# Performance work log

Hardware: AMD Instinct MI355X
Metric: run time of the kernel (lower is better)

The kernel has to match this reference:

```python
import jax, jax.numpy as jnp
import numpy as np

H = 1024      # hidden_size
V = 32000     # output_size (vocab)
L = 512       # max_length (encoder positions)
B = 256       # batch


def setup_inputs() -> dict:
    key = jax.random.key(0)
    ks = jax.random.split(key, 12)
    s = 0.02
    return {
        "input": jax.random.randint(ks[0], (B,), 0, V),
        "hidden": jax.random.normal(ks[1], (1, B, H), jnp.float32),
        "encoder_outputs": jax.random.normal(ks[2], (L, H), jnp.float32),
        # learned params (PyTorch layout: Linear weight is [out, in])
        "emb": jax.random.normal(ks[3], (V, H), jnp.float32) * s,
        "attn_W": jax.random.normal(ks[4], (L, 2 * H), jnp.float32) * s,
        "attn_b": jnp.zeros((L,), jnp.float32),
        "comb_W": jax.random.normal(ks[5], (H, 2 * H), jnp.float32) * s,
        "comb_b": jnp.zeros((H,), jnp.float32),
        "W_ih": jax.random.normal(ks[6], (3 * H, H), jnp.float32) * s,
        "W_hh": jax.random.normal(ks[7], (3 * H, H), jnp.float32) * s,
        "b_ih": jnp.zeros((3 * H,), jnp.float32),
        "b_hh": jnp.zeros((3 * H,), jnp.float32),
        "out_W": jax.random.normal(ks[8], (V, H), jnp.float32) * s,
        "out_b": jnp.zeros((V,), jnp.float32),
    }


def reference(input, hidden, encoder_outputs, emb, attn_W, attn_b,
              comb_W, comb_b, W_ih, W_hh, b_ih, b_hh, out_W, out_b):
    h = hidden[0]                                   # [B,H]
    embedded = emb[input]                           # [B,H] (dropout in eval mode = identity)
    attn_logits = jnp.concatenate([embedded, h], axis=1) @ attn_W.T + attn_b
    attn_weights = jax.nn.softmax(attn_logits, axis=1)        # [B,L]
    attn_applied = attn_weights @ encoder_outputs              # [B,H]
    x = jnp.concatenate([embedded, attn_applied], axis=1) @ comb_W.T + comb_b
    x = jax.nn.relu(x)                                         # [B,H]
    # single-step GRU (PyTorch gate layout: r, z, n)
    gi = x @ W_ih.T + b_ih                                     # [B,3H]
    gh = h @ W_hh.T + b_hh                                     # [B,3H]
    gi_r, gi_z, gi_n = jnp.split(gi, 3, axis=1)
    gh_r, gh_z, gh_n = jnp.split(gh, 3, axis=1)
    r = jax.nn.sigmoid(gi_r + gh_r)
    z = jax.nn.sigmoid(gi_z + gh_z)
    n = jnp.tanh(gi_n + r * gh_n)
    h_new = (1.0 - z) * n + z * h                              # [B,H]
    output = jax.nn.log_softmax(h_new @ out_W.T + out_b, axis=1)  # [B,V]
    return output, h_new[None], attn_weights
```

## Files before the change

kernel.cpp:

```cpp
#include <hip/hip_runtime.h>
#include <hip/hip_bf16.h>
#include <cstdint>

#define DEVI __device__ __forceinline__

typedef __bf16 bf16x8 __attribute__((ext_vector_type(8)));
typedef float  f32x4  __attribute__((ext_vector_type(4)));

constexpr int Hdim = 1024;
constexpr int Vdim = 32000;
constexpr int Ldim = 512;
constexpr int Bdim = 256;

DEVI unsigned short f2bf(float f) {
  __bf16 h = (__bf16)f;
  return __builtin_bit_cast(unsigned short, h);
}

constexpr int FP4 = 36;

__global__ __launch_bounds__(1024, 4)
void gemm_flat5(const unsigned short* __restrict__ A,
                const float* __restrict__ W,
                const float* __restrict__ bias,
                float* __restrict__ C,
                float2* __restrict__ plse)
{
  __shared__ unsigned short lW[4][128 * FP4];

  const int t    = threadIdx.x;
  const int lane = t & 63;
  const int wv   = t >> 6;
  const int r16  = lane & 15;
  const int k8   = (lane >> 4) * 8;
  const int n0   = blockIdx.x * 128;

  const int srow = t >> 3;
  const int stc  = (t & 7) * 4;

  const float*          Wb = W + (size_t)(n0 + srow) * 1024 + stc;
  const unsigned short* Ab = A + (size_t)(wv * 16 + r16) * 1024 + k8;

  f32x4 acc[8];
#pragma unroll
  for (int n = 0; n < 8; ++n)
#pragma unroll
    for (int r = 0; r < 4; ++r) acc[n][r] = 0.f;

  f32x4 w0_, w1_;
  uint4 a0_, a1_, a2_, a3_;

#define LOADW(RW, KT) RW = *reinterpret_cast<const f32x4*>(Wb + (KT) * 32)
#define LOADA(RA, KT) RA = *reinterpret_cast<const uint4*>(Ab + (KT) * 32)

#define STOREW(RW, BUF) do {                                                   \
    ushort4 u_;                                                                \
    u_.x = f2bf(RW[0]); u_.y = f2bf(RW[1]);                                    \
    u_.z = f2bf(RW[2]); u_.w = f2bf(RW[3]);                                    \
    *reinterpret_cast<ushort4*>(&lW[BUF][srow * FP4 + stc]) = u_;              \
  } while (0)

#define COMP(RA, BUF) do {                                                     \
    _Pragma("unroll")                                                          \
    for (int n = 0; n < 8; ++n) {                                              \
      bf16x8 bw_ = *reinterpret_cast<const bf16x8*>(                           \
          &lW[BUF][(n * 16 + r16) * FP4 + k8]);                                \
      acc[n] = __builtin_amdgcn_mfma_f32_16x16x32_bf16(                        \
          __builtin_bit_cast(bf16x8, RA), bw_, acc[n], 0, 0, 0);               \
    }                                                                          \
  } while (0)

  LOADW(w0_, 0); LOADW(w1_, 1);
  LOADA(a0_, 0); LOADA(a1_, 1); LOADA(a2_, 2); LOADA(a3_, 3);
  STOREW(w0_, 0); LOADW(w0_, 2);
  STOREW(w1_, 1); LOADW(w1_, 3);
  __syncthreads();

  for (int kt = 0; kt < 32; kt += 4) {
    COMP(a0_, 0);
    STOREW(w0_, 2);
    { const int kn = (kt + 4 < 32) ? kt + 4 : 31; LOADW(w0_, kn); LOADA(a0_, kn); }
    __syncthreads();

    COMP(a1_, 1);
    STOREW(w1_, 3);
    { const int kn = (kt + 5 < 32) ? kt + 5 : 31; LOADW(w1_, kn); LOADA(a1_, kn); }
    __syncthreads();

    COMP(a2_, 2);
    STOREW(w0_, 0);
    { const int kn = (kt + 6 < 32) ? kt + 6 : 31; LOADW(w0_, kn); LOADA(a2_, kn); }
    __syncthreads();

    COMP(a3_, 3);
    STOREW(w1_, 1);
    { const int kn = (kt + 7 < 32) ? kt + 7 : 31; LOADW(w1_, kn); LOADA(a3_, kn); }
    __syncthreads();
  }

#undef COMP
#undef STOREW
#undef LOADA
#undef LOADW

#pragma unroll
  for (int n = 0; n < 8; ++n) {
    const int col = n0 + n * 16 + r16;
    const float bv = bias[col];
    const int rbase = wv * 16 + (lane >> 4) * 4;
#pragma unroll
    for (int r = 0; r < 4; ++r) {
      const float v = acc[n][r] + bv;
      acc[n][r] = v;
      C[(size_t)(rbase + r) * Vdim + col] = v;
    }
  }
#pragma unroll
  for (int r = 0; r < 4; ++r) {
    float mx = -1e30f;
#pragma unroll
    for (int n = 0; n < 8; ++n) mx = fmaxf(mx, acc[n][r]);
#pragma unroll
    for (int o = 1; o < 16; o <<= 1) mx = fmaxf(mx, __shfl_xor(mx, o, 16));
    float s = 0.f;
#pragma unroll
    for (int n = 0; n < 8; ++n) s += __expf(acc[n][r] - mx);
#pragma unroll
    for (int o = 1; o < 16; o <<= 1) s += __shfl_xor(s, o, 16);
    if (r16 == 0) {
      const int row = wv * 16 + (lane >> 4) * 4 + r;
      plse[(size_t)row * gridDim.x + blockIdx.x] = make_float2(mx, s);
    }
  }
}

struct GP {
  const float* A; const float* W; float* C;
  int K, ldc, ldb, col_off, aact, nsplit, gx;
};

template<bool BTRANS>
__global__ __launch_bounds__(256, 2)
void gemm_multi(GP q0, GP q1, int n0blk)
{
  constexpr int MT = 128, PITCH = 40, ITA = 4, MR = 2;

  __shared__ unsigned short lA[2 * MT * PITCH];
  __shared__ unsigned short lW[2 * 64 * PITCH];

  GP p = q0;
  int id = blockIdx.x;
  if (id >= n0blk) { p = q1; id -= n0blk; }
  const int bx  = id % p.gx;
  const int rem = id / p.gx;
  const int by  = rem & 1;
  const int kz  = rem >> 1;

  const int m0 = by * MT;
  const int n0 = bx * 64;
  const int NK = p.K / (32 * p.nsplit);
  const int kb = kz * NK;

  const int t  = threadIdx.x;
  const int tr = t >> 3;
  const int tc = (t & 7) * 4;

  const float* Af = p.A + (size_t)m0 * p.K;

  const int lane = t & 63;
  const int wv   = t >> 6;
  const int r16  = lane & 15;
  const int k8   = (lane >> 4) * 8;

  f32x4 acc[MR][4];
#pragma unroll
  for (int m = 0; m < MR; ++m)
#pragma unroll
    for (int n = 0; n < 4; ++n)
#pragma unroll
      for (int r = 0; r < 4; ++r) acc[m][n][r] = 0.f;

  struct RS { f32x4 ra[ITA]; f32x4 rw[2]; };

  auto loadT = [&](RS& rg, int kt) {
    const int ko = (kb + kt) * 32;
#pragma unroll
    for (int i = 0; i < ITA; ++i)
      rg.ra[i] = *reinterpret_cast<const f32x4*>(
          Af + (size_t)(tr + 32 * i) * p.K + ko + tc);
    if constexpr (BTRANS) {
      const float* wp = p.W + (size_t)(ko + tr) * p.ldb + n0 + (t & 7) * 8;
      rg.rw[0] = *reinterpret_cast<const f32x4*>(wp);
      rg.rw[1] = *reinterpret_cast<const f32x4*>(wp + 4);
    } else {
#pragma unroll
      for (int i = 0; i < 2; ++i)
        rg.rw[i] = *reinterpret_cast<const f32x4*>(
            p.W + (size_t)(n0 + tr + 32 * i) * p.ldb + ko + tc);
    }
  };

  auto storeT = [&](RS& rg, int bo) {
    unsigned short* sA = &lA[bo * MT * PITCH];
    unsigned short* sW = &lW[bo * 64 * PITCH];
#pragma unroll
    for (int i = 0; i < ITA; ++i) {
      f32x4 v = rg.ra[i];
      if (p.aact) { v[0]=fmaxf(v[0],0.f); v[1]=fmaxf(v[1],0.f);
                    v[2]=fmaxf(v[2],0.f); v[3]=fmaxf(v[3],0.f); }
      ushort4 u;
      u.x = f2bf(v[0]); u.y = f2bf(v[1]); u.z = f2bf(v[2]); u.w = f2bf(v[3]);
      *reinterpret_cast<ushort4*>(&sA[(tr + 32 * i) * PITCH + tc]) = u;
    }
    if constexpr (BTRANS) {
      const int hb = (t & 7) * 8;
#pragma unroll
      for (int j = 0; j < 4; ++j) {
        sW[(hb + j)     * PITCH + tr] = f2bf(rg.rw[0][j]);
        sW[(hb + 4 + j) * PITCH + tr] = f2bf(rg.rw[1][j]);
      }
    } else {
#pragma unroll
      for (int i = 0; i < 2; ++i) {
        f32x4 v = rg.rw[i]; ushort4 u;
        u.x = f2bf(v[0]); u.y = f2bf(v[1]); u.z = f2bf(v[2]); u.w = f2bf(v[3]);
        *reinterpret_cast<ushort4*>(&sW[(tr + 32 * i) * PITCH + tc]) = u;
      }
    }
  };

  auto comp = [&](int bo) {
    const unsigned short* sA = &lA[bo * MT * PITCH];
    const unsigned short* sW = &lW[bo * 64 * PITCH];
    bf16x8 af[MR], bfr[4];
#pragma unroll
    for (int m = 0; m < MR; ++m)
      af[m] = *reinterpret_cast<const bf16x8*>(&sA[(wv * 32 + m * 16 + r16) * PITCH + k8]);
#pragma unroll
    for (int n = 0; n < 4; ++n)
      bfr[n] = *reinterpret_cast<const bf16x8*>(&sW[(n * 16 + r16) * PITCH + k8]);
#pragma unroll
    for (int m = 0; m < MR; ++m)
#pragma unroll
      for (int n = 0; n < 4; ++n)
        acc[m][n] = __builtin_amdgcn_mfma_f32_16x16x32_bf16(af[m], bfr[n], acc[m][n], 0, 0, 0);
  };

#define GB_BARRIER() do { \
    asm volatile("s_waitcnt lgkmcnt(0)" ::: "memory"); \
    __builtin_amdgcn_sched_barrier(0); \
    __builtin_amdgcn_s_barrier(); \
  } while (0)

  RS ra_, rb_;
  loadT(ra_, 0);
  loadT(rb_, 1);
  storeT(ra_, 0);
  GB_BARRIER();

  for (int kt = 0; kt < NK; kt += 2) {
    if (kt + 2 < NK) loadT(ra_, kt + 2);
    comp(0);
    storeT(rb_, 1);
    GB_BARRIER();
    if (kt + 3 < NK) loadT(rb_, kt + 3);
    comp(1);
    if (kt + 2 < NK) {
      storeT(ra_, 0);
      GB_BARRIER();
    }
  }
#undef GB_BARRIER

#pragma unroll
  for (int n = 0; n < 4; ++n) {
    const int col = n0 + n * 16 + r16;
#pragma unroll
    for (int m = 0; m < MR; ++m) {
      const int rbase = m0 + wv * 32 + m * 16 + (lane >> 4) * 4;
#pragma unroll
      for (int r = 0; r < 4; ++r)
        atomicAdd(&p.C[(size_t)(rbase + r) * p.ldc + p.col_off + col],
                  acc[m][n][r]);
    }
  }
}

__global__ void prep_kernel(const int* __restrict__ ids, const float* __restrict__ hid,
                            const float* __restrict__ emb,
                            const float* __restrict__ attn_b, const float* __restrict__ comb_b,
                            const float* __restrict__ b_ih, const float* __restrict__ b_hh,
                            float* __restrict__ X0, float* __restrict__ X1,
                            float* __restrict__ alog, float* __restrict__ xact,
                            float* __restrict__ gi, float* __restrict__ gh)
{
  const int b = blockIdx.x, t = threadIdx.x;
  const int row = ids[b];
  f32x4 e = *reinterpret_cast<const f32x4*>(emb + (size_t)row * Hdim + t * 4);
  *reinterpret_cast<f32x4*>(X0 + (size_t)b * 2048 + t * 4) = e;
  *reinterpret_cast<f32x4*>(X1 + (size_t)b * 2048 + t * 4) = e;
  f32x4 h = *reinterpret_cast<const f32x4*>(hid + (size_t)b * Hdim + t * 4);
  *reinterpret_cast<f32x4*>(X0 + (size_t)b * 2048 + 1024 + t * 4) = h;
  f32x4 z4 = {0.f, 0.f, 0.f, 0.f};
  *reinterpret_cast<f32x4*>(X1 + (size_t)b * 2048 + 1024 + t * 4) = z4;
  if (t < 128)
    *reinterpret_cast<f32x4*>(alog + (size_t)b * Ldim + t * 4) =
        *reinterpret_cast<const f32x4*>(attn_b + t * 4);
  *reinterpret_cast<f32x4*>(xact + (size_t)b * Hdim + t * 4) =
      *reinterpret_cast<const f32x4*>(comb_b + t * 4);
#pragma unroll
  for (int i = 0; i < 3; ++i) {
    *reinterpret_cast<f32x4*>(gi + (size_t)b * 3072 + i * 1024 + t * 4) =
        *reinterpret_cast<const f32x4*>(b_ih + i * 1024 + t * 4);
    *reinterpret_cast<f32x4*>(gh + (size_t)b * 3072 + i * 1024 + t * 4) =
        *reinterpret_cast<const f32x4*>(b_hh + i * 1024 + t * 4);
  }
}

__global__ void attn_softmax_kernel(const float* __restrict__ logits, float* __restrict__ wout)
{
  __shared__ float red[256];
  const int b = blockIdx.x, t = threadIdx.x;
  const float x0 = logits[b * Ldim + t];
  const float x1 = logits[b * Ldim + 256 + t];
  red[t] = fmaxf(x0, x1); __syncthreads();
  for (int o = 128; o > 0; o >>= 1) { if (t < o) red[t] = fmaxf(red[t], red[t + o]); __syncthreads(); }
  const float m = red[0]; __syncthreads();
  const float e0 = __expf(x0 - m), e1 = __expf(x1 - m);
  red[t] = e0 + e1; __syncthreads();
  for (int o = 128; o > 0; o >>= 1) { if (t < o) red[t] += red[t + o]; __syncthreads(); }
  const float inv = 1.f / red[0];
  wout[b * Ldim + t]       = e0 * inv;
  wout[b * Ldim + 256 + t] = e1 * inv;
}

DEVI float sigm(float x) { return 1.f / (1.f + __expf(-x)); }

__global__ void gru_kernel(const float* __restrict__ gi, const float* __restrict__ gh,
                           const float* __restrict__ hin,
                           float* __restrict__ hnew, unsigned short* __restrict__ hnbf)
{
  const int idx = blockIdx.x * 256 + threadIdx.x;
  const int b = idx >> 10, j = idx & 1023;
  const float* gib = gi + (size_t)b * 3072;
  const float* ghb = gh + (size_t)b * 3072;
  const float r = sigm(gib[j] + ghb[j]);
  const float z = sigm(gib[1024 + j] + ghb[1024 + j]);
  const float n = tanhf(gib[2048 + j] + r * ghb[2048 + j]);
  const float h = hin[idx];
  const float hn = (1.f - z) * n + z * h;
  hnew[idx] = hn;
  hnbf[idx] = f2bf(hn);
}

__global__ void lsm_sub2(const float2* __restrict__ part, int npart,
                         float* __restrict__ out)
{
  __shared__ float rm[256], rs[256];
  const int b = blockIdx.x >> 3, c = blockIdx.x & 7;
  const int t = threadIdx.x;
  float m = -1e30f, s = 0.f;
  for (int j = t; j < npart; j += 256) {
    const float2 p = part[(size_t)b * npart + j];
    const float nm = fmaxf(m, p.x);
    s = s * __expf(m - nm) + p.y * __expf(p.x - nm);
    m = nm;
  }
  rm[t] = m; rs[t] = s; __syncthreads();
  for (int o = 128; o > 0; o >>= 1) {
    if (t < o) {
      const float m2 = rm[t + o], s2 = rs[t + o];
      const float nm = fmaxf(rm[t], m2);
      rs[t] = rs[t] * __expf(rm[t] - nm) + s2 * __expf(m2 - nm);
      rm[t] = nm;
    }
    __syncthreads();
  }
  const float lse = rm[0] + __logf(rs[0]);
  f32x4* row4 = reinterpret_cast<f32x4*>(out + (size_t)b * Vdim) + c * 1000;
  for (int i = t; i < 1000; i += 256) {
    f32x4 x = row4[i];
    x[0] -= lse; x[1] -= lse; x[2] -= lse; x[3] -= lse;
    row4[i] = x;
  }
}

extern "C" void kernel_launch(void* const* d_in, const int* in_sizes, int n_in,
                              void* d_out, int out_size, void* d_ws, size_t ws_size,
                              hipStream_t stream)
{
  (void)in_sizes; (void)n_in; (void)out_size; (void)ws_size;

  const int*   ids    = (const int*)  d_in[0];
  const float* hid    = (const float*)d_in[1];
  const float* enc    = (const float*)d_in[2];
  const float* emb    = (const float*)d_in[3];
  const float* attn_W = (const float*)d_in[4];
  const float* attn_b = (const float*)d_in[5];
  const float* comb_W = (const float*)d_in[6];
  const float* comb_b = (const float*)d_in[7];
  const float* W_ih   = (const float*)d_in[8];
  const float* W_hh   = (const float*)d_in[9];
  const float* b_ih   = (const float*)d_in[10];
  const float* b_hh   = (const float*)d_in[11];
  const float* out_W  = (const float*)d_in[12];
  const float* out_b  = (const float*)d_in[13];

  float* out_logits = (float*)d_out;
  float* out_h      = out_logits + (size_t)Bdim * Vdim;
  float* out_attw   = out_h + (size_t)Bdim * Hdim;

  char* w = (char*)d_ws;
  float* X0   = (float*)w; w += (size_t)Bdim * 2048 * 4;
  float* X1   = (float*)w; w += (size_t)Bdim * 2048 * 4;
  float* alog = (float*)w; w += (size_t)Bdim * Ldim * 4;
  float* xact = (float*)w; w += (size_t)Bdim * Hdim * 4;
  float* gi   = (float*)w; w += (size_t)Bdim * 3 * Hdim * 4;
  float* gh   = (float*)w; w += (size_t)Bdim * 3 * Hdim * 4;
  unsigned short* hnbf = (unsigned short*)w; w += (size_t)Bdim * Hdim * 2;
  float2* plse = (float2*)w; w += (size_t)Bdim * (Vdim / 128) * 8;

  prep_kernel<<<Bdim, 256, 0, stream>>>(ids, hid, emb, attn_b, comb_b, b_ih, b_hh,
                                        X0, X1, alog, xact, gi, gh);

  {
    GP p0 = { X0,  attn_W, alog, 2048, Ldim,     2048, 0, 0, 8,  Ldim / 64 };
    GP p1 = { hid, W_hh,   gh,   1024, 3 * Hdim, 1024, 0, 0, 4,  3 * Hdim / 64 };
    const int n0blk = p0.gx * 2 * p0.nsplit;
    const int nblk  = n0blk + p1.gx * 2 * p1.nsplit;
    gemm_multi<false><<<nblk, 256, 0, stream>>>(p0, p1, n0blk);
  }

  attn_softmax_kernel<<<Bdim, 256, 0, stream>>>(alog, out_attw);

  {
    GP p0 = { out_attw, enc, X1, 512, 2048, Hdim, 1024, 0, 4, Hdim / 64 };
    const int nblk = p0.gx * 2 * p0.nsplit;
    gemm_multi<true><<<nblk, 256, 0, stream>>>(p0, p0, nblk);
  }

  {
    GP p0 = { X1, comb_W, xact, 2048, Hdim, 2048, 0, 0, 8, Hdim / 64 };
    const int nblk = p0.gx * 2 * p0.nsplit;
    gemm_multi<false><<<nblk, 256, 0, stream>>>(p0, p0, nblk);
  }

  {
    GP p0 = { xact, W_ih, gi, 1024, 3 * Hdim, 1024, 0, 1, 4, 3 * Hdim / 64 };
    const int nblk = p0.gx * 2 * p0.nsplit;
    gemm_multi<false><<<nblk, 256, 0, stream>>>(p0, p0, nblk);
  }

  gru_kernel<<<Bdim * Hdim / 256, 256, 0, stream>>>(gi, gh, hid, out_h, hnbf);

  gemm_flat5<<<Vdim / 128, 1024, 0, stream>>>(hnbf, out_W, out_b, out_logits, plse);

  lsm_sub2<<<Bdim * 8, 256, 0, stream>>>(plse, Vdim / 128, out_logits);
}
```

Measured before the change: 115.6 us.

## Fuse log-softmax normalization into output GEMM via grid-wide barrier

The output-projection GEMM now keeps its logits in registers, publishes per-block max/sum partials, waits at a software grid barrier built on an atomic counter, has 16 blocks reduce the row LSE values, waits at a second barrier, and then writes the normalized log-probabilities directly. This drops the separate lsm_sub2 kernel, which re-read and re-wrote the whole 256x32000 logits buffer, and saves a launch. In exchange it adds a memset launch and two spin barriers, and it depends on all 250 blocks of 1024 threads being resident at the same time (launch bounds relaxed to 2 blocks per CU), otherwise the kernel can deadlock.

After: 192.2 us. 66.3% more time.

```diff
diff --git a/kernel.cpp b/kernel.cpp
--- a/kernel.cpp
+++ b/kernel.cpp
@@ -18,13 +18,16 @@
 }
 
 constexpr int FP4 = 36;
-
-__global__ __launch_bounds__(1024, 4)
-void gemm_flat5(const unsigned short* __restrict__ A,
+constexpr int GF_GRID = Vdim / 128;
+
+__global__ __launch_bounds__(1024, 2)
+void gemm_flat6(const unsigned short* __restrict__ A,
                 const float* __restrict__ W,
                 const float* __restrict__ bias,
                 float* __restrict__ C,
-                float2* __restrict__ plse)
+                float2* __restrict__ plse,
+                float* __restrict__ lse,
+                unsigned int* __restrict__ ctr)
 {
   __shared__ unsigned short lW[4][128 * FP4];
 
@@ -105,16 +108,11 @@
 
 #pragma unroll
   for (int n = 0; n < 8; ++n) {
-    const int col = n0 + n * 16 + r16;
-    const float bv = bias[col];
-    const int rbase = wv * 16 + (lane >> 4) * 4;
-#pragma unroll
-    for (int r = 0; r < 4; ++r) {
-      const float v = acc[n][r] + bv;
-      acc[n][r] = v;
-      C[(size_t)(rbase + r) * Vdim + col] = v;
-    }
-  }
+    const float bv = bias[n0 + n * 16 + r16];
+#pragma unroll
+    for (int r = 0; r < 4; ++r) acc[n][r] += bv;
+  }
+  const int rbase = wv * 16 + (lane >> 4) * 4;
 #pragma unroll
   for (int r = 0; r < 4; ++r) {
     float mx = -1e30f;
@@ -127,10 +125,63 @@
     for (int n = 0; n < 8; ++n) s += __expf(acc[n][r] - mx);
 #pragma unroll
     for (int o = 1; o < 16; o <<= 1) s += __shfl_xor(s, o, 16);
-    if (r16 == 0) {
-      const int row = wv * 16 + (lane >> 4) * 4 + r;
-      plse[(size_t)row * gridDim.x + blockIdx.x] = make_float2(mx, s);
-    }
+    if (r16 == 0)
+      plse[(size_t)(rbase + r) * GF_GRID + blockIdx.x] = make_float2(mx, s);
+  }
+
+  __syncthreads();
+  if (t == 0) {
+    __threadfence();
+    atomicAdd(&ctr[0], 1u);
+    while (__hip_atomic_load(&ctr[0], __ATOMIC_ACQUIRE,
+                             __HIP_MEMORY_SCOPE_AGENT) < (unsigned)GF_GRID) {
+      __builtin_amdgcn_s_sleep(1);
+    }
+  }
+  __syncthreads();
+  (void)__hip_atomic_load(&ctr[0], __ATOMIC_ACQUIRE, __HIP_MEMORY_SCOPE_AGENT);
+
+  if (blockIdx.x < 16) {
+    const int row = blockIdx.x * 16 + wv;
+    float m = -1e30f, s = 0.f;
+    for (int j = lane; j < GF_GRID; j += 64) {
+      const float2 p = plse[(size_t)row * GF_GRID + j];
+      const float nm = fmaxf(m, p.x);
+      s = s * __expf(m - nm) + p.y * __expf(p.x - nm);
+      m = nm;
+    }
+#pragma unroll
+    for (int o = 1; o < 64; o <<= 1) {
+      const float m2 = __shfl_xor(m, o);
+      const float s2 = __shfl_xor(s, o);
+      const float nm = fmaxf(m, m2);
+      s = s * __expf(m - nm) + s2 * __expf(m2 - nm);
+      m = nm;
+    }
+    if (lane == 0) lse[row] = m + __logf(s);
+  }
+
+  __syncthreads();
+  if (t == 0) {
+    __threadfence();
+    if (blockIdx.x < 16) atomicAdd(&ctr[1], 1u);
+    while (__hip_atomic_load(&ctr[1], __ATOMIC_ACQUIRE,
+                             __HIP_MEMORY_SCOPE_AGENT) < 16u) {
+      __builtin_amdgcn_s_sleep(1);
+    }
+  }
+  __syncthreads();
+  (void)__hip_atomic_load(&ctr[1], __ATOMIC_ACQUIRE, __HIP_MEMORY_SCOPE_AGENT);
+
+  float lr[4];
+#pragma unroll
+  for (int r = 0; r < 4; ++r) lr[r] = lse[rbase + r];
+#pragma unroll
+  for (int n = 0; n < 8; ++n) {
+    const int col = n0 + n * 16 + r16;
+#pragma unroll
+    for (int r = 0; r < 4; ++r)
+      C[(size_t)(rbase + r) * Vdim + col] = acc[n][r] - lr[r];
   }
 }
 
@@ -353,38 +404,6 @@
   hnbf[idx] = f2bf(hn);
 }
 
-__global__ void lsm_sub2(const float2* __restrict__ part, int npart,
-                         float* __restrict__ out)
-{
-  __shared__ float rm[256], rs[256];
-  const int b = blockIdx.x >> 3, c = blockIdx.x & 7;
-  const int t = threadIdx.x;
-  float m = -1e30f, s = 0.f;
-  for (int j = t; j < npart; j += 256) {
-    const float2 p = part[(size_t)b * npart + j];
-    const float nm = fmaxf(m, p.x);
-    s = s * __expf(m - nm) + p.y * __expf(p.x - nm);
-    m = nm;
-  }
-  rm[t] = m; rs[t] = s; __syncthreads();
-  for (int o = 128; o > 0; o >>= 1) {
-    if (t < o) {
-      const float m2 = rm[t + o], s2 = rs[t + o];
-      const float nm = fmaxf(rm[t], m2);
-      rs[t] = rs[t] * __expf(rm[t] - nm) + s2 * __expf(m2 - nm);
-      rm[t] = nm;
-    }
-    __syncthreads();
-  }
-  const float lse = rm[0] + __logf(rs[0]);
-  f32x4* row4 = reinterpret_cast<f32x4*>(out + (size_t)b * Vdim) + c * 1000;
-  for (int i = t; i < 1000; i += 256) {
-    f32x4 x = row4[i];
-    x[0] -= lse; x[1] -= lse; x[2] -= lse; x[3] -= lse;
-    row4[i] = x;
-  }
-}
-
 extern "C" void kernel_launch(void* const* d_in, const int* in_sizes, int n_in,
                               void* d_out, int out_size, void* d_ws, size_t ws_size,
                               hipStream_t stream)
@@ -418,7 +437,9 @@
   float* gi   = (float*)w; w += (size_t)Bdim * 3 * Hdim * 4;
   float* gh   = (float*)w; w += (size_t)Bdim * 3 * Hdim * 4;
   unsigned short* hnbf = (unsigned short*)w; w += (size_t)Bdim * Hdim * 2;
-  float2* plse = (float2*)w; w += (size_t)Bdim * (Vdim / 128) * 8;
+  float2* plse = (float2*)w; w += (size_t)Bdim * GF_GRID * 8;
+  float* lse   = (float*)w;  w += (size_t)Bdim * 4;
+  unsigned int* ctr = (unsigned int*)w; w += 8;
 
   prep_kernel<<<Bdim, 256, 0, stream>>>(ids, hid, emb, attn_b, comb_b, b_ih, b_hh,
                                         X0, X1, alog, xact, gi, gh);
@@ -453,7 +474,7 @@
 
   gru_kernel<<<Bdim * Hdim / 256, 256, 0, stream>>>(gi, gh, hid, out_h, hnbf);
 
-  gemm_flat5<<<Vdim / 128, 1024, 0, stream>>>(hnbf, out_W, out_b, out_logits, plse);
-
-  lsm_sub2<<<Bdim * 8, 256, 0, stream>>>(plse, Vdim / 128, out_logits);
-}
+  hipMemsetAsync(ctr, 0, 2 * sizeof(unsigned int), stream);
+  gemm_flat6<<<GF_GRID, 1024, 0, stream>>>(hnbf, out_W, out_b, out_logits,
+                                           plse, lse, ctr);
+}
```

## Warp-specialize output GEMM with producer waves staging full-K weight chunks

Applied to the files above, without the earlier changes.

The vocab-projection GEMM is split into producer and consumer halves. Threads 512-1023 load 32-row by full-K chunks of the fp32 weights, convert them to bf16 and store them into a double-buffered, XOR-swizzled LDS tile. Threads 0-511 each compute a 32x128 output tile, with two MFMA row groups sharing each B fragment. This replaces the prior scheme where every wave both staged and computed with a barrier every 32-K step, cutting barriers from about 32 to 4. In exchange only half the waves issue MFMAs, LDS use grows to 128 KB per block, and the A operand is re-read from global memory for each of the 4 chunks.

Measured after the change: 233.9 us. 2.02x slower.

```diff
diff --git a/kernel.cpp b/kernel.cpp
--- a/kernel.cpp
+++ b/kernel.cpp
@@ -12,124 +12,133 @@
 constexpr int Ldim = 512;
 constexpr int Bdim = 256;
 
+constexpr int GF_GRID = Vdim / 128;
+
 DEVI unsigned short f2bf(float f) {
   __bf16 h = (__bf16)f;
   return __builtin_bit_cast(unsigned short, h);
 }
 
-constexpr int FP4 = 36;
-
 __global__ __launch_bounds__(1024, 4)
-void gemm_flat5(const unsigned short* __restrict__ A,
+void gemm_flat7(const unsigned short* __restrict__ A,
                 const float* __restrict__ W,
                 const float* __restrict__ bias,
                 float* __restrict__ C,
                 float2* __restrict__ plse)
 {
-  __shared__ unsigned short lW[4][128 * FP4];
+  __shared__ unsigned short lW[2][32 * 1024];
 
   const int t    = threadIdx.x;
   const int lane = t & 63;
   const int wv   = t >> 6;
   const int r16  = lane & 15;
-  const int k8   = (lane >> 4) * 8;
+  const int kq   = lane >> 4;
+  const int k8   = kq * 8;
   const int n0   = blockIdx.x * 128;
-
-  const int srow = t >> 3;
-  const int stc  = (t & 7) * 4;
-
-  const float*          Wb = W + (size_t)(n0 + srow) * 1024 + stc;
-  const unsigned short* Ab = A + (size_t)(wv * 16 + r16) * 1024 + k8;
-
-  f32x4 acc[8];
-#pragma unroll
-  for (int n = 0; n < 8; ++n)
-#pragma unroll
-    for (int r = 0; r < 4; ++r) acc[n][r] = 0.f;
-
-  f32x4 w0_, w1_;
-  uint4 a0_, a1_, a2_, a3_;
-
-#define LOADW(RW, KT) RW = *reinterpret_cast<const f32x4*>(Wb + (KT) * 32)
-#define LOADA(RA, KT) RA = *reinterpret_cast<const uint4*>(Ab + (KT) * 32)
-
-#define STOREW(RW, BUF) do {                                                   \
-    ushort4 u_;                                                                \
-    u_.x = f2bf(RW[0]); u_.y = f2bf(RW[1]);                                    \
-    u_.z = f2bf(RW[2]); u_.w = f2bf(RW[3]);                                    \
-    *reinterpret_cast<ushort4*>(&lW[BUF][srow * FP4 + stc]) = u_;              \
-  } while (0)
-
-#define COMP(RA, BUF) do {                                                     \
-    _Pragma("unroll")                                                          \
-    for (int n = 0; n < 8; ++n) {                                              \
-      bf16x8 bw_ = *reinterpret_cast<const bf16x8*>(                           \
-          &lW[BUF][(n * 16 + r16) * FP4 + k8]);                                \
-      acc[n] = __builtin_amdgcn_mfma_f32_16x16x32_bf16(                        \
-          __builtin_bit_cast(bf16x8, RA), bw_, acc[n], 0, 0, 0);               \
-    }                                                                          \
-  } while (0)
-
-  LOADW(w0_, 0); LOADW(w1_, 1);
-  LOADA(a0_, 0); LOADA(a1_, 1); LOADA(a2_, 2); LOADA(a3_, 3);
-  STOREW(w0_, 0); LOADW(w0_, 2);
-  STOREW(w1_, 1); LOADW(w1_, 3);
+  const int swz  = (r16 & 7) << 4;
+
+  auto pstage = [&](int ch, int buf) {
+    const int pt = t - 512;
+    const float* src = W + ((size_t)n0 + ch * 32) * 1024;
+    uint4 sreg[16];
+#pragma unroll
+    for (int j = 0; j < 16; ++j)
+      sreg[j] = *reinterpret_cast<const uint4*>(src + (j * 512 + pt) * 4);
+    const int u   = pt & 255;
+    const int rh  = pt >> 8;
+#pragma unroll
+    for (int j = 0; j < 16; ++j) {
+      const int row = j * 2 + rh;
+      f32x4 v = __builtin_bit_cast(f32x4, sreg[j]);
+      ushort4 o;
+      o.x = f2bf(v[0]); o.y = f2bf(v[1]); o.z = f2bf(v[2]); o.w = f2bf(v[3]);
+      *reinterpret_cast<ushort4*>(
+          (char*)&lW[buf][0] + ((row * 2048 + u * 8) ^ ((row & 7) << 4))) = o;
+    }
+  };
+
+  f32x4 acc[2][8];
+#pragma unroll
+  for (int m = 0; m < 2; ++m)
+#pragma unroll
+    for (int n = 0; n < 8; ++n)
+#pragma unroll
+      for (int r = 0; r < 4; ++r) acc[m][n][r] = 0.f;
+
+  const unsigned short* Ab0 = A + (size_t)(wv * 32 + r16) * 1024 + k8;
+  const unsigned short* Ab1 = Ab0 + (size_t)16 * 1024;
+
+  auto ccompute = [&](int c, int buf) {
+    const char* lb = (const char*)&lW[buf][0];
+    uint4 aw[8];
+#pragma unroll
+    for (int q = 0; q < 4; ++q) {
+      aw[q * 2 + 0] = *reinterpret_cast<const uint4*>(Ab0 + q * 32);
+      aw[q * 2 + 1] = *reinterpret_cast<const uint4*>(Ab1 + q * 32);
+    }
+#pragma unroll
+    for (int kt = 0; kt < 32; ++kt) {
+      const int kb = kt * 64 + kq * 16;
+      bf16x8 b0 = *reinterpret_cast<const bf16x8*>(
+          lb + ((r16 * 2048 + kb) ^ swz));
+      bf16x8 b1 = *reinterpret_cast<const bf16x8*>(
+          lb + (((r16 + 16) * 2048 + kb) ^ swz));
+      bf16x8 a0 = __builtin_bit_cast(bf16x8, aw[(kt & 3) * 2 + 0]);
+      bf16x8 a1 = __builtin_bit_cast(bf16x8, aw[(kt & 3) * 2 + 1]);
+      acc[0][2 * c + 0] = __builtin_amdgcn_mfma_f32_16x16x32_bf16(a0, b0, acc[0][2 * c + 0], 0, 0, 0);
+      acc[0][2 * c + 1] = __builtin_amdgcn_mfma_f32_16x16x32_bf16(a0, b1, acc[0][2 * c + 1], 0, 0, 0);
+      acc[1][2 * c + 0] = __builtin_amdgcn_mfma_f32_16x16x32_bf16(a1, b0, acc[1][2 * c + 0], 0, 0, 0);
+      acc[1][2 * c + 1] = __builtin_amdgcn_mfma_f32_16x16x32_bf16(a1, b1, acc[1][2 * c + 1], 0, 0, 0);
+      if (kt + 4 < 32) {
+        aw[(kt & 3) * 2 + 0] = *reinterpret_cast<const uint4*>(Ab0 + (kt + 4) * 32);
+        aw[(kt & 3) * 2 + 1] = *reinterpret_cast<const uint4*>(Ab1 + (kt + 4) * 32);
+      }
+    }
+  };
+
+  if (t >= 512) pstage(0, 0);
   __syncthreads();
 
-  for (int kt = 0; kt < 32; kt += 4) {
-    COMP(a0_, 0);
-    STOREW(w0_, 2);
-    { const int kn = (kt + 4 < 32) ? kt + 4 : 31; LOADW(w0_, kn); LOADA(a0_, kn); }
+#pragma unroll
+  for (int c = 0; c < 4; ++c) {
+    if (t >= 512) {
+      if (c < 3) pstage(c + 1, (c + 1) & 1);
+    } else {
+      ccompute(c, c & 1);
+    }
     __syncthreads();
-
-    COMP(a1_, 1);
-    STOREW(w1_, 3);
-    { const int kn = (kt + 5 < 32) ? kt + 5 : 31; LOADW(w1_, kn); LOADA(a1_, kn); }
-    __syncthreads();
-
-    COMP(a2_, 2);
-    STOREW(w0_, 0);
-    { const int kn = (kt + 6 < 32) ? kt + 6 : 31; LOADW(w0_, kn); LOADA(a2_, kn); }
-    __syncthreads();
-
-    COMP(a3_, 3);
-    STOREW(w1_, 1);
-    { const int kn = (kt + 7 < 32) ? kt + 7 : 31; LOADW(w1_, kn); LOADA(a3_, kn); }
-    __syncthreads();
-  }
-
-#undef COMP
-#undef STOREW
-#undef LOADA
-#undef LOADW
-
-#pragma unroll
-  for (int n = 0; n < 8; ++n) {
-    const int col = n0 + n * 16 + r16;
-    const float bv = bias[col];
-    const int rbase = wv * 16 + (lane >> 4) * 4;
+  }
+
+  if (t >= 512) return;
+
+#pragma unroll
+  for (int m = 0; m < 2; ++m) {
+    const int rbase = wv * 32 + m * 16 + kq * 4;
+#pragma unroll
+    for (int n = 0; n < 8; ++n) {
+      const int col = n0 + n * 16 + r16;
+      const float bv = bias[col];
+#pragma unroll
+      for (int r = 0; r < 4; ++r) {
+        const float v = acc[m][n][r] + bv;
+        acc[m][n][r] = v;
+        C[(size_t)(rbase + r) * Vdim + col] = v;
+      }
+    }
 #pragma unroll
     for (int r = 0; r < 4; ++r) {
-      const float v = acc[n][r] + bv;
-      acc[n][r] = v;
-      C[(size_t)(rbase + r) * Vdim + col] = v;
-    }
-  }
-#pragma unroll
-  for (int r = 0; r < 4; ++r) {
-    float mx = -1e30f;
-#pragma unroll
-    for (int n = 0; n < 8; ++n) mx = fmaxf(mx, acc[n][r]);
-#pragma unroll
-    for (int o = 1; o < 16; o <<= 1) mx = fmaxf(mx, __shfl_xor(mx, o, 16));
-    float s = 0.f;
-#pragma unroll
-    for (int n = 0; n < 8; ++n) s += __expf(acc[n][r] - mx);
-#pragma unroll
-    for (int o = 1; o < 16; o <<= 1) s += __shfl_xor(s, o, 16);
-    if (r16 == 0) {
-      const int row = wv * 16 + (lane >> 4) * 4 + r;
-      plse[(size_t)row * gridDim.x + blockIdx.x] = make_float2(mx, s);
+      float mx = -1e30f;
+#pragma unroll
+      for (int n = 0; n < 8; ++n) mx = fmaxf(mx, acc[m][n][r]);
+#pragma unroll
+      for (int o = 1; o < 16; o <<= 1) mx = fmaxf(mx, __shfl_xor(mx, o, 16));
+      float s = 0.f;
+#pragma unroll
+      for (int n = 0; n < 8; ++n) s += __expf(acc[m][n][r] - mx);
+#pragma unroll
+      for (int o = 1; o < 16; o <<= 1) s += __shfl_xor(s, o, 16);
+      if (r16 == 0)
+        plse[(size_t)(rbase + r) * GF_GRID + blockIdx.x] = make_float2(mx, s);
     }
   }
 }
@@ -418,7 +427,7 @@
   float* gi   = (float*)w; w += (size_t)Bdim * 3 * Hdim * 4;
   float* gh   = (float*)w; w += (size_t)Bdim * 3 * Hdim * 4;
   unsigned short* hnbf = (unsigned short*)w; w += (size_t)Bdim * Hdim * 2;
-  float2* plse = (float2*)w; w += (size_t)Bdim * (Vdim / 128) * 8;
+  float2* plse = (float2*)w; w += (size_t)Bdim * GF_GRID * 8;
 
   prep_kernel<<<Bdim, 256, 0, stream>>>(ids, hid, emb, attn_b, comb_b, b_ih, b_hh,
                                         X0, X1, alog, xact, gi, gh);
@@ -453,7 +462,7 @@
 
   gru_kernel<<<Bdim * Hdim / 256, 256, 0, stream>>>(gi, gh, hid, out_h, hnbf);
 
-  gemm_flat5<<<Vdim / 128, 1024, 0, stream>>>(hnbf, out_W, out_b, out_logits, plse);
-
-  lsm_sub2<<<Bdim * 8, 256, 0, stream>>>(plse, Vdim / 128, out_logits);
-}
+  gemm_flat7<<<GF_GRID, 1024, 0, stream>>>(hnbf, out_W, out_b, out_logits, plse);
+
+  lsm_sub2<<<Bdim * 8, 256, 0, stream>>>(plse, GF_GRID, out_logits);
+}
```
